# Optimization experiments

Hardware: AMD Instinct MI355X
Metric: run time of the kernel (lower is better)

The kernel has to match this reference:

```python
import jax, jax.numpy as jnp
import numpy as np

DIM = 1024
HEADS = 16
DIM_HEAD = DIM // HEADS
SCALE = DIM_HEAD ** -0.5
LN_EPS = 1e-5


def setup_inputs() -> dict:
    key = jax.random.key(0)
    ks = jax.random.split(key, 10)
    b, n, m = 2, 2048, 2048
    s = 0.02
    return {
        "x": jax.random.normal(ks[0], (b, n, DIM), jnp.float32),
        "context": jax.random.normal(ks[1], (b, m, DIM), jnp.float32),
        "alibi": jax.random.normal(ks[2], (HEADS, n, m), jnp.float32),
        "Wq": jax.random.normal(ks[3], (DIM, DIM), jnp.float32) * s,
        "Wk": jax.random.normal(ks[4], (DIM, DIM), jnp.float32) * s,
        "Wv": jax.random.normal(ks[5], (DIM, DIM), jnp.float32) * s,
        "Wo": jax.random.normal(ks[6], (DIM, DIM), jnp.float32) * s,
        "bo": jnp.zeros((DIM,), jnp.float32),
        "ln_w": jnp.ones((DIM,), jnp.float32),
        "ln_b": jnp.zeros((DIM,), jnp.float32),
    }


def _layernorm(t, w, b):
    mu = jnp.mean(t, axis=-1, keepdims=True)
    var = jnp.var(t, axis=-1, keepdims=True)
    return (t - mu) * jax.lax.rsqrt(var + LN_EPS) * w + b


def reference(x, context, alibi, Wq, Wk, Wv, Wo, bo, ln_w, ln_b):
    xn = _layernorm(x, ln_w, ln_b)
    cn = _layernorm(context, ln_w, ln_b)
    # torch Linear: y = x @ W.T
    q = xn @ Wq.T
    k = cn @ Wk.T
    v = cn @ Wv.T
    b, n, _ = q.shape
    m = k.shape[1]
    # b n (h d) -> b h n d
    q = q.reshape(b, n, HEADS, DIM_HEAD).transpose(0, 2, 1, 3)
    k = k.reshape(b, m, HEADS, DIM_HEAD).transpose(0, 2, 1, 3)
    v = v.reshape(b, m, HEADS, DIM_HEAD).transpose(0, 2, 1, 3)
    scores = jnp.einsum("bhid,bhjd->bhij", q, k) * SCALE + alibi
    attn = jax.nn.softmax(scores, axis=-1)
    out = jnp.einsum("bhij,bhjd->bhid", attn, v)
    out = out.transpose(0, 2, 1, 3).reshape(b, n, HEADS * DIM_HEAD)
    return out @ Wo.T + bo
```

## Files before the change

### kernel.cpp

```cpp
#include <hip/hip_runtime.h>

#define DIM 1024
#define HEADS 16
#define DHEAD 64
#define LN_EPS 1e-5f
#define SCALE 0.125f

typedef _Float16 h8 __attribute__((ext_vector_type(8)));
typedef _Float16 h4 __attribute__((ext_vector_type(4)));
typedef _Float16 h2 __attribute__((ext_vector_type(2)));
typedef float f32x4 __attribute__((ext_vector_type(4)));

__device__ __forceinline__ float wave_sum(float v) {
#pragma unroll
  for (int o = 32; o > 0; o >>= 1) v += __shfl_xor(v, o, 64);
  return v;
}

__global__ __launch_bounds__(256) void cast_kernel(const float* __restrict__ src,
                                                   _Float16* __restrict__ dst) {
  int idx = blockIdx.x * 256 + threadIdx.x;
  float4 f = ((const float4*)src)[idx];
  h4 o;
  o[0] = (_Float16)f.x; o[1] = (_Float16)f.y;
  o[2] = (_Float16)f.z; o[3] = (_Float16)f.w;
  ((h4*)dst)[idx] = o;
}

__global__ __launch_bounds__(256) void ln_f16(const float* __restrict__ in,
                                              _Float16* __restrict__ out,
                                              const float* __restrict__ w,
                                              const float* __restrict__ b) {
  int row = blockIdx.x;
  const float4* rp = (const float4*)(in + (size_t)row * DIM);
  float4 v = rp[threadIdx.x];
  float s = v.x + v.y + v.z + v.w;
  float ss = fmaf(v.x, v.x, fmaf(v.y, v.y, fmaf(v.z, v.z, v.w * v.w)));
  s = wave_sum(s);
  ss = wave_sum(ss);
  __shared__ float red[8];
  int wid = threadIdx.x >> 6, lane = threadIdx.x & 63;
  if (lane == 0) { red[wid] = s; red[4 + wid] = ss; }
  __syncthreads();
  s = red[0] + red[1] + red[2] + red[3];
  ss = red[4] + red[5] + red[6] + red[7];
  float mu = s * (1.0f / DIM);
  float var = ss * (1.0f / DIM) - mu * mu;
  float inv = rsqrtf(var + LN_EPS);
  float4 wv = ((const float4*)w)[threadIdx.x];
  float4 bv = ((const float4*)b)[threadIdx.x];
  h4 o;
  o[0] = (_Float16)((v.x - mu) * inv * wv.x + bv.x);
  o[1] = (_Float16)((v.y - mu) * inv * wv.y + bv.y);
  o[2] = (_Float16)((v.z - mu) * inv * wv.z + bv.z);
  o[3] = (_Float16)((v.w - mu) * inv * wv.w + bv.w);
  *(h4*)(out + (size_t)row * DIM + 4 * threadIdx.x) = o;
}

template <bool HALF_OUT>
__global__ __launch_bounds__(256) void gemm_nt_f16(const _Float16* __restrict__ A,
                                                   const _Float16* __restrict__ W,
                                                   void* __restrict__ C,
                                                   const float* __restrict__ bias) {
  __shared__ _Float16 As[128][40];
  __shared__ _Float16 Ws[64][40];
  int tid = threadIdx.x;
  int w = tid >> 6, lane = tid & 63;
  int quad = lane >> 4, l15 = lane & 15;
  int wr = w >> 1, wc = w & 1;
  int rowBase = blockIdx.y * 128;
  int colBase = blockIdx.x * 64;

  f32x4 acc[4][2] = {};

  int ar = tid >> 1, asel = tid & 1;
  int wrow = tid >> 2, wsel = tid & 3;

  for (int k0 = 0; k0 < DIM; k0 += 32) {
    const _Float16* asrc = A + (size_t)(rowBase + ar) * DIM + k0 + asel * 16;
    h8 a0 = *(const h8*)asrc;
    h8 a1 = *(const h8*)(asrc + 8);
    *(h8*)&As[ar][asel * 16] = a0;
    *(h8*)&As[ar][asel * 16 + 8] = a1;
    const _Float16* wsrc = W + (size_t)(colBase + wrow) * DIM + k0 + wsel * 8;
    h8 w0 = *(const h8*)wsrc;
    *(h8*)&Ws[wrow][wsel * 8] = w0;
    __syncthreads();

    h8 af[4];
#pragma unroll
    for (int mg = 0; mg < 4; mg++)
      af[mg] = *(const h8*)&As[wr * 64 + mg * 16 + l15][quad * 8];
    h8 bf[2];
#pragma unroll
    for (int ng = 0; ng < 2; ng++)
      bf[ng] = *(const h8*)&Ws[wc * 32 + ng * 16 + l15][quad * 8];
#pragma unroll
    for (int mg = 0; mg < 4; mg++)
#pragma unroll
      for (int ng = 0; ng < 2; ng++)
        acc[mg][ng] = __builtin_amdgcn_mfma_f32_16x16x32_f16(af[mg], bf[ng], acc[mg][ng], 0, 0, 0);
    __syncthreads();
  }

#pragma unroll
  for (int mg = 0; mg < 4; mg++) {
#pragma unroll
    for (int ng = 0; ng < 2; ng++) {
      int n = colBase + wc * 32 + ng * 16 + l15;
      float bv = 0.f;
      if (!HALF_OUT && bias) bv = bias[n];
#pragma unroll
      for (int reg = 0; reg < 4; reg++) {
        int m = rowBase + wr * 64 + mg * 16 + quad * 4 + reg;
        if (HALF_OUT)
          ((_Float16*)C)[(size_t)m * DIM + n] = (_Float16)acc[mg][ng][reg];
        else
          ((float*)C)[(size_t)m * DIM + n] = acc[mg][ng][reg] + bv;
      }
    }
  }
}

__global__ __launch_bounds__(256) void attn_mfma(const _Float16* __restrict__ q,
                                                 const _Float16* __restrict__ k,
                                                 const _Float16* __restrict__ v,
                                                 const float* __restrict__ alibi,
                                                 _Float16* __restrict__ out) {
  __shared__ _Float16 Ks[64][72];
  __shared__ _Float16 Vs[64][72];
  __shared__ _Float16 Ps[4][16][72];

  int tid = threadIdx.x;
  int w = tid >> 6, lane = tid & 63;
  int quad = lane >> 4, l15 = lane & 15;
  int qbase = blockIdx.x * 64;
  int h = blockIdx.y, bi = blockIdx.z;

  const _Float16* kg = k + (size_t)bi * 2048 * DIM + h * DHEAD;
  const _Float16* vg = v + (size_t)bi * 2048 * DIM + h * DHEAD;
  const float* ap = alibi + (size_t)h * 2048 * 2048;

  const _Float16* qp = q + (size_t)(bi * 2048 + qbase + w * 16 + l15) * DIM + h * DHEAD;
  h8 qf[2];
  qf[0] = *(const h8*)(qp + quad * 8);
  qf[1] = *(const h8*)(qp + 32 + quad * 8);

  float m_i[4], l_i[4];
#pragma unroll
  for (int r = 0; r < 4; r++) { m_i[r] = -INFINITY; l_i[r] = 0.f; }
  f32x4 o_acc[4] = {};

  int kr = tid >> 2, kq = tid & 3;
  int vp = tid & 31, vd = tid >> 5;

  for (int kb = 0; kb < 2048; kb += 64) {
    {
      const _Float16* src = kg + (size_t)(kb + kr) * DIM + kq * 16;
      h8 k0 = *(const h8*)src;
      h8 k1 = *(const h8*)(src + 8);
      *(h8*)&Ks[kr][kq * 16] = k0;
      *(h8*)&Ks[kr][kq * 16 + 8] = k1;
    }
    {
      const _Float16* sv0 = vg + (size_t)(kb + 2 * vp) * DIM + vd * 8;
      h8 va = *(const h8*)sv0;
      h8 vb = *(const h8*)(sv0 + DIM);
#pragma unroll
      for (int i = 0; i < 8; i++) {
        h2 pr; pr[0] = va[i]; pr[1] = vb[i];
        *(h2*)&Vs[vd * 8 + i][2 * vp] = pr;
      }
    }
    __syncthreads();

    f32x4 s_acc[4] = {};
#pragma unroll
    for (int ng = 0; ng < 4; ng++) {
#pragma unroll
      for (int ks = 0; ks < 2; ks++) {
        h8 bf = *(const h8*)&Ks[ng * 16 + l15][ks * 32 + quad * 8];
        s_acc[ng] = __builtin_amdgcn_mfma_f32_16x16x32_f16(qf[ks], bf, s_acc[ng], 0, 0, 0);
      }
    }

    int iq0 = qbase + w * 16 + quad * 4;
    float alpha[4];
    float p_val[4][4];
#pragma unroll
    for (int r = 0; r < 4; r++) {
      float sv[4];
      float mx = -INFINITY;
#pragma unroll
      for (int ng = 0; ng < 4; ng++) {
        sv[ng] = fmaf(s_acc[ng][r], SCALE, ap[(size_t)(iq0 + r) * 2048 + kb + ng * 16 + l15]);
        mx = fmaxf(mx, sv[ng]);
      }
#pragma unroll
      for (int off = 8; off > 0; off >>= 1) mx = fmaxf(mx, __shfl_xor(mx, off, 64));
      float mn = fmaxf(m_i[r], mx);
      alpha[r] = __expf(m_i[r] - mn);
      float rs = 0.f;
#pragma unroll
      for (int ng = 0; ng < 4; ng++) {
        p_val[ng][r] = __expf(sv[ng] - mn);
        rs += p_val[ng][r];
      }
#pragma unroll
      for (int off = 8; off > 0; off >>= 1) rs += __shfl_xor(rs, off, 64);
      l_i[r] = l_i[r] * alpha[r] + rs;
      m_i[r] = mn;
    }
#pragma unroll
    for (int ng = 0; ng < 4; ng++)
#pragma unroll
      for (int r = 0; r < 4; r++)
        Ps[w][quad * 4 + r][ng * 16 + l15] = (_Float16)p_val[ng][r];
    __syncthreads();

#pragma unroll
    for (int ngd = 0; ngd < 4; ngd++)
#pragma unroll
      for (int r = 0; r < 4; r++) o_acc[ngd][r] *= alpha[r];

    h8 pf[2];
    pf[0] = *(const h8*)&Ps[w][l15][quad * 8];
    pf[1] = *(const h8*)&Ps[w][l15][32 + quad * 8];
#pragma unroll
    for (int ngd = 0; ngd < 4; ngd++) {
#pragma unroll
      for (int ks = 0; ks < 2; ks++) {
        h8 vf = *(const h8*)&Vs[ngd * 16 + l15][ks * 32 + quad * 8];
        o_acc[ngd] = __builtin_amdgcn_mfma_f32_16x16x32_f16(pf[ks], vf, o_acc[ngd], 0, 0, 0);
      }
    }
    __syncthreads();
  }

#pragma unroll
  for (int ngd = 0; ngd < 4; ngd++) {
#pragma unroll
    for (int r = 0; r < 4; r++) {
      int iq = qbase + w * 16 + quad * 4 + r;
      out[(size_t)(bi * 2048 + iq) * DIM + h * DHEAD + ngd * 16 + l15] =
          (_Float16)(o_acc[ngd][r] / l_i[r]);
    }
  }
}

extern "C" void kernel_launch(void* const* d_in, const int* in_sizes, int n_in,
                              void* d_out, int out_size, void* d_ws, size_t ws_size,
                              hipStream_t stream) {
  const float* x = (const float*)d_in[0];
  const float* context = (const float*)d_in[1];
  const float* alibi = (const float*)d_in[2];
  const float* Wq = (const float*)d_in[3];
  const float* Wk = (const float*)d_in[4];
  const float* Wv = (const float*)d_in[5];
  const float* Wo = (const float*)d_in[6];
  const float* bo = (const float*)d_in[7];
  const float* ln_w = (const float*)d_in[8];
  const float* ln_b = (const float*)d_in[9];
  float* out = (float*)d_out;

  const size_t WSZ = (size_t)DIM * DIM;
  const size_t MSZ = (size_t)4096 * DIM;
  _Float16* ws16 = (_Float16*)d_ws;
  _Float16* wq_h = ws16;
  _Float16* wk_h = wq_h + WSZ;
  _Float16* wv_h = wk_h + WSZ;
  _Float16* wo_h = wv_h + WSZ;
  _Float16* xnh = wo_h + WSZ;
  _Float16* cnh = xnh + MSZ;
  _Float16* qh = cnh + MSZ;
  _Float16* kh = qh + MSZ;
  _Float16* vh = kh + MSZ;
  _Float16* aoh = vh + MSZ;

  cast_kernel<<<1024, 256, 0, stream>>>(Wq, wq_h);
  cast_kernel<<<1024, 256, 0, stream>>>(Wk, wk_h);
  cast_kernel<<<1024, 256, 0, stream>>>(Wv, wv_h);
  cast_kernel<<<1024, 256, 0, stream>>>(Wo, wo_h);

  ln_f16<<<4096, 256, 0, stream>>>(x, xnh, ln_w, ln_b);
  ln_f16<<<4096, 256, 0, stream>>>(context, cnh, ln_w, ln_b);

  dim3 gg(DIM / 64, 4096 / 128);
  gemm_nt_f16<true><<<gg, 256, 0, stream>>>(xnh, wq_h, qh, nullptr);
  gemm_nt_f16<true><<<gg, 256, 0, stream>>>(cnh, wk_h, kh, nullptr);
  gemm_nt_f16<true><<<gg, 256, 0, stream>>>(cnh, wv_h, vh, nullptr);

  dim3 ag(2048 / 64, HEADS, 2);
  attn_mfma<<<ag, 256, 0, stream>>>(qh, kh, vh, alibi, aoh);

  gemm_nt_f16<false><<<gg, 256, 0, stream>>>(aoh, wo_h, out, bo);
}
```

Before: 576.5 us.

## Merge launches, use direct global-to-LDS loads, enlarge attention blocks, use exp2 softmax

Merges the four weight casts into one launch and both layernorms into one. K and V projections now share a single GEMM launch. The GEMMs load tiles straight from global memory into LDS with global_load_lds, using a k-major layout and a K-step of 64. Attention now runs 512-thread blocks covering 128 queries, prefetches alibi into registers, folds scale·log2e into Q so it can use exp2, and computes the row sums with an MFMA against a ones vector instead of shuffles. It also drops one barrier per tile. The aim is less launch overhead and fewer LDS and VALU instructions, at the cost of more register pressure and the risk of LDS bank conflicts from the unpadded layouts.

```diff
diff --git a/kernel.cpp b/kernel.cpp
--- a/kernel.cpp
+++ b/kernel.cpp
@@ -1,38 +1,59 @@
 #include <hip/hip_runtime.h>
+#include <stdint.h>
 
 #define DIM 1024
 #define HEADS 16
 #define DHEAD 64
 #define LN_EPS 1e-5f
 #define SCALE 0.125f
+#define LOG2E 1.44269504089f
 
 typedef _Float16 h8 __attribute__((ext_vector_type(8)));
 typedef _Float16 h4 __attribute__((ext_vector_type(4)));
 typedef _Float16 h2 __attribute__((ext_vector_type(2)));
 typedef float f32x4 __attribute__((ext_vector_type(4)));
 
+typedef __attribute__((address_space(1))) void* as1p;
+typedef __attribute__((address_space(3))) void* as3p;
+
+__device__ __forceinline__ void gl_lds16(const void* g, void* l) {
+  __builtin_amdgcn_global_load_lds((as1p)g, (as3p)l, 16, 0, 0);
+}
+
 __device__ __forceinline__ float wave_sum(float v) {
 #pragma unroll
   for (int o = 32; o > 0; o >>= 1) v += __shfl_xor(v, o, 64);
   return v;
 }
 
-__global__ __launch_bounds__(256) void cast_kernel(const float* __restrict__ src,
-                                                   _Float16* __restrict__ dst) {
-  int idx = blockIdx.x * 256 + threadIdx.x;
-  float4 f = ((const float4*)src)[idx];
+__global__ __launch_bounds__(256) void cast4_kernel(const float* __restrict__ W0,
+                                                    const float* __restrict__ W1,
+                                                    const float* __restrict__ W2,
+                                                    const float* __restrict__ W3,
+                                                    _Float16* __restrict__ dst) {
+  int gi = blockIdx.x * 256 + threadIdx.x;
+  int wsel = gi >> 18;
+  int li = gi & 0x3FFFF;
+  const float* s = W0;
+  if (wsel == 1) s = W1;
+  else if (wsel == 2) s = W2;
+  else if (wsel == 3) s = W3;
+  float4 f = ((const float4*)s)[li];
   h4 o;
   o[0] = (_Float16)f.x; o[1] = (_Float16)f.y;
   o[2] = (_Float16)f.z; o[3] = (_Float16)f.w;
-  ((h4*)dst)[idx] = o;
-}
-
-__global__ __launch_bounds__(256) void ln_f16(const float* __restrict__ in,
+  ((h4*)dst)[gi] = o;
+}
+
+__global__ __launch_bounds__(256) void ln_f16(const float* __restrict__ x,
+                                              const float* __restrict__ context,
                                               _Float16* __restrict__ out,
                                               const float* __restrict__ w,
                                               const float* __restrict__ b) {
   int row = blockIdx.x;
-  const float4* rp = (const float4*)(in + (size_t)row * DIM);
+  const float* src = (row < 4096) ? x : context;
+  int srow = row & 4095;
+  const float4* rp = (const float4*)(src + (size_t)srow * DIM);
   float4 v = rp[threadIdx.x];
   float s = v.x + v.y + v.z + v.w;
   float ss = fmaf(v.x, v.x, fmaf(v.y, v.y, fmaf(v.z, v.z, v.w * v.w)));
@@ -57,84 +78,111 @@
   *(h4*)(out + (size_t)row * DIM + 4 * threadIdx.x) = o;
 }
 
-template <bool HALF_OUT>
-__global__ __launch_bounds__(256) void gemm_nt_f16(const _Float16* __restrict__ A,
-                                                   const _Float16* __restrict__ W,
-                                                   void* __restrict__ C,
-                                                   const float* __restrict__ bias) {
-  __shared__ _Float16 As[128][40];
-  __shared__ _Float16 Ws[64][40];
+template <int OUT_MODE>
+__device__ __forceinline__ void gemm_core(const _Float16* __restrict__ A,
+                                          const _Float16* __restrict__ W,
+                                          void* __restrict__ C,
+                                          const float* __restrict__ bias,
+                                          int rowBase, int colBase) {
+  __shared__ _Float16 As[128 * 64];
+  __shared__ _Float16 Bs[64 * 64];
   int tid = threadIdx.x;
   int w = tid >> 6, lane = tid & 63;
   int quad = lane >> 4, l15 = lane & 15;
   int wr = w >> 1, wc = w & 1;
-  int rowBase = blockIdx.y * 128;
-  int colBase = blockIdx.x * 64;
-
   f32x4 acc[4][2] = {};
 
-  int ar = tid >> 1, asel = tid & 1;
-  int wrow = tid >> 2, wsel = tid & 3;
-
-  for (int k0 = 0; k0 < DIM; k0 += 32) {
-    const _Float16* asrc = A + (size_t)(rowBase + ar) * DIM + k0 + asel * 16;
-    h8 a0 = *(const h8*)asrc;
-    h8 a1 = *(const h8*)(asrc + 8);
-    *(h8*)&As[ar][asel * 16] = a0;
-    *(h8*)&As[ar][asel * 16 + 8] = a1;
-    const _Float16* wsrc = W + (size_t)(colBase + wrow) * DIM + k0 + wsel * 8;
-    h8 w0 = *(const h8*)wsrc;
-    *(h8*)&Ws[wrow][wsel * 8] = w0;
+  for (int k0 = 0; k0 < DIM; k0 += 64) {
+#pragma unroll
+    for (int l = 0; l < 4; l++) {
+      int id = l * 256 + tid;
+      int row = id & 127, c = id >> 7;
+      gl_lds16(A + (size_t)(rowBase + row) * DIM + k0 + c * 8,
+               &As[(l * 256 + w * 64) * 8]);
+    }
+#pragma unroll
+    for (int l = 0; l < 2; l++) {
+      int id = l * 256 + tid;
+      int row = id & 63, c = id >> 6;
+      gl_lds16(W + (size_t)(colBase + row) * DIM + k0 + c * 8,
+               &Bs[(l * 256 + w * 64) * 8]);
+    }
     __syncthreads();
 
-    h8 af[4];
+    h8 af[4][2], bf[2][2];
+#pragma unroll
+    for (int ks = 0; ks < 2; ks++) {
+#pragma unroll
+      for (int mg = 0; mg < 4; mg++)
+        af[mg][ks] = *(const h8*)&As[((ks * 4 + quad) * 128 + wr * 64 + mg * 16 + l15) * 8];
+#pragma unroll
+      for (int ng = 0; ng < 2; ng++)
+        bf[ng][ks] = *(const h8*)&Bs[((ks * 4 + quad) * 64 + wc * 32 + ng * 16 + l15) * 8];
+    }
 #pragma unroll
     for (int mg = 0; mg < 4; mg++)
-      af[mg] = *(const h8*)&As[wr * 64 + mg * 16 + l15][quad * 8];
-    h8 bf[2];
-#pragma unroll
-    for (int ng = 0; ng < 2; ng++)
-      bf[ng] = *(const h8*)&Ws[wc * 32 + ng * 16 + l15][quad * 8];
-#pragma unroll
-    for (int mg = 0; mg < 4; mg++)
 #pragma unroll
       for (int ng = 0; ng < 2; ng++)
-        acc[mg][ng] = __builtin_amdgcn_mfma_f32_16x16x32_f16(af[mg], bf[ng], acc[mg][ng], 0, 0, 0);
+#pragma unroll
+        for (int ks = 0; ks < 2; ks++)
+          acc[mg][ng] = __builtin_amdgcn_mfma_f32_16x16x32_f16(af[mg][ks], bf[ng][ks], acc[mg][ng], 0, 0, 0);
     __syncthreads();
   }
 
 #pragma unroll
-  for (int mg = 0; mg < 4; mg++) {
+  for (int mg = 0; mg < 4; mg++)
 #pragma unroll
     for (int ng = 0; ng < 2; ng++) {
-      int n = colBase + wc * 32 + ng * 16 + l15;
-      float bv = 0.f;
-      if (!HALF_OUT && bias) bv = bias[n];
-#pragma unroll
-      for (int reg = 0; reg < 4; reg++) {
-        int m = rowBase + wr * 64 + mg * 16 + quad * 4 + reg;
-        if (HALF_OUT)
-          ((_Float16*)C)[(size_t)m * DIM + n] = (_Float16)acc[mg][ng][reg];
+      int ccol = colBase + wc * 32 + ng * 16 + l15;
+      float bv = (OUT_MODE == 1) ? bias[ccol] : 0.f;
+#pragma unroll
+      for (int r = 0; r < 4; r++) {
+        int crow = rowBase + wr * 64 + mg * 16 + quad * 4 + r;
+        if (OUT_MODE == 0)
+          ((_Float16*)C)[(size_t)crow * DIM + ccol] = (_Float16)acc[mg][ng][r];
         else
-          ((float*)C)[(size_t)m * DIM + n] = acc[mg][ng][reg] + bv;
-      }
-    }
-  }
-}
-
-__global__ __launch_bounds__(256) void attn_mfma(const _Float16* __restrict__ q,
-                                                 const _Float16* __restrict__ k,
-                                                 const _Float16* __restrict__ v,
-                                                 const float* __restrict__ alibi,
-                                                 _Float16* __restrict__ out) {
-  __shared__ _Float16 Ks[64][72];
+          ((float*)C)[(size_t)crow * DIM + ccol] = acc[mg][ng][r] + bv;
+      }
+    }
+}
+
+__global__ __launch_bounds__(256) void gemm_f16(const _Float16* __restrict__ A,
+                                                const _Float16* __restrict__ W,
+                                                _Float16* __restrict__ C) {
+  gemm_core<0>(A, W, C, nullptr, blockIdx.y * 128, blockIdx.x * 64);
+}
+
+__global__ __launch_bounds__(256) void gemm_kv(const _Float16* __restrict__ A,
+                                               const _Float16* __restrict__ Wk,
+                                               const _Float16* __restrict__ Wv,
+                                               _Float16* __restrict__ Ck,
+                                               _Float16* __restrict__ Cv) {
+  int sel = blockIdx.x >> 4;
+  const _Float16* W = sel ? Wv : Wk;
+  _Float16* C = sel ? Cv : Ck;
+  gemm_core<0>(A, W, C, nullptr, blockIdx.y * 128, (blockIdx.x & 15) * 64);
+}
+
+__global__ __launch_bounds__(256) void gemm_out(const _Float16* __restrict__ A,
+                                                const _Float16* __restrict__ W,
+                                                float* __restrict__ C,
+                                                const float* __restrict__ bias) {
+  gemm_core<1>(A, W, C, bias, blockIdx.y * 128, blockIdx.x * 64);
+}
+
+__global__ __launch_bounds__(512, 4) void attn_mfma(const _Float16* __restrict__ q,
+                                                    const _Float16* __restrict__ k,
+                                                    const _Float16* __restrict__ v,
+                                                    const float* __restrict__ alibi,
+                                                    _Float16* __restrict__ out) {
+  __shared__ _Float16 Ks[64 * 64];
   __shared__ _Float16 Vs[64][72];
-  __shared__ _Float16 Ps[4][16][72];
+  __shared__ _Float16 Ps[8][16][72];
 
   int tid = threadIdx.x;
   int w = tid >> 6, lane = tid & 63;
   int quad = lane >> 4, l15 = lane & 15;
-  int qbase = blockIdx.x * 64;
+  int qbase = blockIdx.x * 128;
   int h = blockIdx.y, bi = blockIdx.z;
 
   const _Float16* kg = k + (size_t)bi * 2048 * DIM + h * DHEAD;
@@ -145,107 +193,110 @@
   h8 qf[2];
   qf[0] = *(const h8*)(qp + quad * 8);
   qf[1] = *(const h8*)(qp + 32 + quad * 8);
-
-  float m_i[4], l_i[4];
-#pragma unroll
-  for (int r = 0; r < 4; r++) { m_i[r] = -INFINITY; l_i[r] = 0.f; }
+  const _Float16 qs = (_Float16)(SCALE * LOG2E);
+  qf[0] *= qs;
+  qf[1] *= qs;
+
+  h8 ones;
+#pragma unroll
+  for (int i = 0; i < 8; i++) ones[i] = (_Float16)1.0f;
+
+  float m_i[4] = {-INFINITY, -INFINITY, -INFINITY, -INFINITY};
+  f32x4 l_acc = {0.f, 0.f, 0.f, 0.f};
   f32x4 o_acc[4] = {};
 
-  int kr = tid >> 2, kq = tid & 3;
+  int kkey = tid & 63, kc = tid >> 6;
   int vp = tid & 31, vd = tid >> 5;
 
   for (int kb = 0; kb < 2048; kb += 64) {
+    float av[4][4];
+#pragma unroll
+    for (int r = 0; r < 4; r++) {
+      const float* arow = ap + (size_t)(qbase + w * 16 + quad * 4 + r) * 2048 + kb;
+#pragma unroll
+      for (int ng = 0; ng < 4; ng++) av[r][ng] = arow[ng * 16 + l15];
+    }
+    gl_lds16(kg + (size_t)(kb + kkey) * DIM + kc * 8, &Ks[(w * 64) * 8]);
     {
-      const _Float16* src = kg + (size_t)(kb + kr) * DIM + kq * 16;
-      h8 k0 = *(const h8*)src;
-      h8 k1 = *(const h8*)(src + 8);
-      *(h8*)&Ks[kr][kq * 16] = k0;
-      *(h8*)&Ks[kr][kq * 16 + 8] = k1;
-    }
-    {
-      const _Float16* sv0 = vg + (size_t)(kb + 2 * vp) * DIM + vd * 8;
-      h8 va = *(const h8*)sv0;
-      h8 vb = *(const h8*)(sv0 + DIM);
-#pragma unroll
-      for (int i = 0; i < 8; i++) {
-        h2 pr; pr[0] = va[i]; pr[1] = vb[i];
-        *(h2*)&Vs[vd * 8 + i][2 * vp] = pr;
+      const _Float16* sv0 = vg + (size_t)(kb + 2 * vp) * DIM + vd * 4;
+      h4 va = *(const h4*)sv0;
+      h4 vb = *(const h4*)(sv0 + DIM);
+#pragma unroll
+      for (int i = 0; i < 4; i++) {
+        h2 pr;
+        pr[0] = va[i];
+        pr[1] = vb[i];
+        *(h2*)&Vs[vd * 4 + i][2 * vp] = pr;
       }
     }
     __syncthreads();
 
     f32x4 s_acc[4] = {};
 #pragma unroll
-    for (int ng = 0; ng < 4; ng++) {
+    for (int ng = 0; ng < 4; ng++)
 #pragma unroll
       for (int ks = 0; ks < 2; ks++) {
-        h8 bf = *(const h8*)&Ks[ng * 16 + l15][ks * 32 + quad * 8];
-        s_acc[ng] = __builtin_amdgcn_mfma_f32_16x16x32_f16(qf[ks], bf, s_acc[ng], 0, 0, 0);
-      }
-    }
-
-    int iq0 = qbase + w * 16 + quad * 4;
-    float alpha[4];
-    float p_val[4][4];
+        h8 bfr = *(const h8*)&Ks[((ks * 4 + quad) * 64 + ng * 16 + l15) * 8];
+        s_acc[ng] = __builtin_amdgcn_mfma_f32_16x16x32_f16(qf[ks], bfr, s_acc[ng], 0, 0, 0);
+      }
+
+    float sv[4][4], mloc[4];
 #pragma unroll
     for (int r = 0; r < 4; r++) {
-      float sv[4];
-      float mx = -INFINITY;
+      float m0 = -INFINITY;
 #pragma unroll
       for (int ng = 0; ng < 4; ng++) {
-        sv[ng] = fmaf(s_acc[ng][r], SCALE, ap[(size_t)(iq0 + r) * 2048 + kb + ng * 16 + l15]);
-        mx = fmaxf(mx, sv[ng]);
-      }
-#pragma unroll
-      for (int off = 8; off > 0; off >>= 1) mx = fmaxf(mx, __shfl_xor(mx, off, 64));
-      float mn = fmaxf(m_i[r], mx);
-      alpha[r] = __expf(m_i[r] - mn);
-      float rs = 0.f;
-#pragma unroll
-      for (int ng = 0; ng < 4; ng++) {
-        p_val[ng][r] = __expf(sv[ng] - mn);
-        rs += p_val[ng][r];
-      }
-#pragma unroll
-      for (int off = 8; off > 0; off >>= 1) rs += __shfl_xor(rs, off, 64);
-      l_i[r] = l_i[r] * alpha[r] + rs;
+        sv[r][ng] = fmaf(av[r][ng], LOG2E, s_acc[ng][r]);
+        m0 = fmaxf(m0, sv[r][ng]);
+      }
+      mloc[r] = m0;
+    }
+#pragma unroll
+    for (int off = 8; off > 0; off >>= 1)
+#pragma unroll
+      for (int r = 0; r < 4; r++) mloc[r] = fmaxf(mloc[r], __shfl_xor(mloc[r], off, 64));
+    float alphav[4];
+#pragma unroll
+    for (int r = 0; r < 4; r++) {
+      float mn = fmaxf(m_i[r], mloc[r]);
+      alphav[r] = exp2f(m_i[r] - mn);
       m_i[r] = mn;
     }
 #pragma unroll
-    for (int ng = 0; ng < 4; ng++)
-#pragma unroll
-      for (int r = 0; r < 4; r++)
-        Ps[w][quad * 4 + r][ng * 16 + l15] = (_Float16)p_val[ng][r];
-    __syncthreads();
-
+    for (int r = 0; r < 4; r++)
+#pragma unroll
+      for (int ng = 0; ng < 4; ng++)
+        Ps[w][quad * 4 + r][ng * 16 + l15] = (_Float16)exp2f(sv[r][ng] - m_i[r]);
+#pragma unroll
+    for (int r = 0; r < 4; r++) l_acc[r] *= alphav[r];
 #pragma unroll
     for (int ngd = 0; ngd < 4; ngd++)
 #pragma unroll
-      for (int r = 0; r < 4; r++) o_acc[ngd][r] *= alpha[r];
+      for (int r = 0; r < 4; r++) o_acc[ngd][r] *= alphav[r];
 
     h8 pf[2];
     pf[0] = *(const h8*)&Ps[w][l15][quad * 8];
     pf[1] = *(const h8*)&Ps[w][l15][32 + quad * 8];
-#pragma unroll
-    for (int ngd = 0; ngd < 4; ngd++) {
+    l_acc = __builtin_amdgcn_mfma_f32_16x16x32_f16(pf[0], ones, l_acc, 0, 0, 0);
+    l_acc = __builtin_amdgcn_mfma_f32_16x16x32_f16(pf[1], ones, l_acc, 0, 0, 0);
+#pragma unroll
+    for (int ngd = 0; ngd < 4; ngd++)
 #pragma unroll
       for (int ks = 0; ks < 2; ks++) {
         h8 vf = *(const h8*)&Vs[ngd * 16 + l15][ks * 32 + quad * 8];
         o_acc[ngd] = __builtin_amdgcn_mfma_f32_16x16x32_f16(pf[ks], vf, o_acc[ngd], 0, 0, 0);
       }
-    }
     __syncthreads();
   }
 
 #pragma unroll
-  for (int ngd = 0; ngd < 4; ngd++) {
+  for (int ngd = 0; ngd < 4; ngd++)
 #pragma unroll
     for (int r = 0; r < 4; r++) {
       int iq = qbase + w * 16 + quad * 4 + r;
       out[(size_t)(bi * 2048 + iq) * DIM + h * DHEAD + ngd * 16 + l15] =
-          (_Float16)(o_acc[ngd][r] / l_i[r]);
-    }
-  }
+          (_Float16)(o_acc[ngd][r] / l_acc[r]);
+    }
 }
 
 extern "C" void kernel_launch(void* const* d_in, const int* in_sizes, int n_in,
@@ -277,21 +328,16 @@
   _Float16* vh = kh + MSZ;
   _Float16* aoh = vh + MSZ;
 
-  cast_kernel<<<1024, 256, 0, stream>>>(Wq, wq_h);
-  cast_kernel<<<1024, 256, 0, stream>>>(Wk, wk_h);
-  cast_kernel<<<1024, 256, 0, stream>>>(Wv, wv_h);
-  cast_kernel<<<1024, 256, 0, stream>>>(Wo, wo_h);
-
-  ln_f16<<<4096, 256, 0, stream>>>(x, xnh, ln_w, ln_b);
-  ln_f16<<<4096, 256, 0, stream>>>(context, cnh, ln_w, ln_b);
-
-  dim3 gg(DIM / 64, 4096 / 128);
-  gemm_nt_f16<true><<<gg, 256, 0, stream>>>(xnh, wq_h, qh, nullptr);
-  gemm_nt_f16<true><<<gg, 256, 0, stream>>>(cnh, wk_h, kh, nullptr);
-  gemm_nt_f16<true><<<gg, 256, 0, stream>>>(cnh, wv_h, vh, nullptr);
-
-  dim3 ag(2048 / 64, HEADS, 2);
-  attn_mfma<<<ag, 256, 0, stream>>>(qh, kh, vh, alibi, aoh);
-
-  gemm_nt_f16<false><<<gg, 256, 0, stream>>>(aoh, wo_h, out, bo);
-}
+  cast4_kernel<<<4096, 256, 0, stream>>>(Wq, Wk, Wv, Wo, wq_h);
+  ln_f16<<<8192, 256, 0, stream>>>(x, context, xnh, ln_w, ln_b);
+
+  dim3 gq(16, 32);
+  gemm_f16<<<gq, 256, 0, stream>>>(xnh, wq_h, qh);
+  dim3 gkv(32, 32);
+  gemm_kv<<<gkv, 256, 0, stream>>>(cnh, wk_h, wv_h, kh, vh);
+
+  dim3 ag(16, HEADS, 2);
+  attn_mfma<<<ag, 512, 0, stream>>>(qh, kh, vh, alibi, aoh);
+
+  gemm_out<<<gq, 256, 0, stream>>>(aoh, wo_h, out, bo);
+}
```

New measurement: 572.5 us. Within noise of the previous version (-0.7%).
